# Performance work log

Hardware: AMD Instinct MI355X
Metric: run time of the kernel (lower is better)

Reference implementation:

```python
import jax, jax.numpy as jnp
import numpy as np

N, T, CUT = 64, 2, 25.0            # atoms, atom types, cutoff radius
ED = [3, 32, 64, 128]              # embedding MLP dims (input 3)
LD = [384, 256, 256, 128, 3]       # per-atom MLP dims (input 3*E)
P = T * (T + 1) // 2               # number of unordered type pairs
M = 27 * N                         # periodic images


def setup_inputs() -> dict:
    key = jax.random.key(0)
    ks = jax.random.split(key, 16)
    x = jax.random.uniform(ks[0], (N, 3), jnp.float32) * 10.0
    lattice = 10.0 * jnp.eye(3, dtype=jnp.float32)
    atom_types = (jnp.arange(N) % T).astype(jnp.int32)

    def lin(k, shape, fan_in):
        return jax.random.normal(k, shape, jnp.float32) / np.sqrt(fan_in)

    inp = {"x": x, "lattice": lattice}
    for i in range(3):
        inp[f"We{i+1}"] = lin(ks[1 + i], (P, ED[i], ED[i + 1]), ED[i])
        inp[f"be{i+1}"] = jnp.zeros((P, ED[i + 1]), jnp.float32)
    for i in range(4):
        inp[f"Wl{i+1}"] = lin(ks[5 + i], (N, LD[i], LD[i + 1]), LD[i])
        inp[f"bl{i+1}"] = jnp.zeros((N, LD[i + 1]), jnp.float32)
    inp["atom_types"] = atom_types
    return inp


def reference(x, lattice, We1, be1, We2, be2, We3, be3,
              Wl1, bl1, Wl2, bl2, Wl3, bl3, Wl4, bl4, atom_types):
    act = jax.nn.leaky_relu  # slope 0.01, matches nn.LeakyReLU default
    idx = jnp.arange(-1, 2, dtype=x.dtype)
    # (i,j,k) combos in the same loop order as torch (i slowest, k fastest)
    combos = jnp.stack(jnp.meshgrid(idx, idx, idx, indexing="ij"), -1).reshape(27, 3)
    x_ext = (x[None, :, :] + (combos @ lattice)[:, None, :]).reshape(M, 3)  # [M,3]
    # the in-place subtraction in torch telescopes: at step n, x_ext = x_ext0 - x_ext0[n]
    rel = x_ext[None, :, :] - x_ext[:N, None, :]                    # [N,M,3]
    dist = jnp.linalg.norm(rel, axis=-1)                            # [N,M]
    mask = dist <= CUT
    rank = jnp.cumsum(mask, axis=1) - 1
    # torch removes POSITION n of the compacted neighbor list -> rank == n
    keep = (mask & (rank != jnp.arange(N)[:, None])).astype(x.dtype)  # [N,M]

    types_ext = jnp.tile(atom_types, 27)                            # [M]
    lo = jnp.minimum(atom_types[:, None], types_ext[None, :])
    hi = jnp.maximum(atom_types[:, None], types_ext[None, :])
    pid = lo * T - (lo * (lo - 1)) // 2 + (hi - lo)                 # [N,M] pair-type id

    # run all P pair-type embedding MLPs on every candidate edge, then route
    h = act(jnp.einsum("nmi,pio->pnmo", rel, We1) + be1[:, None, None, :])
    h = act(jnp.einsum("pnmi,pio->pnmo", h, We2) + be2[:, None, None, :])
    h = act(jnp.einsum("pnmi,pio->pnmo", h, We3) + be3[:, None, None, :])
    g = h[pid, jnp.arange(N)[:, None], jnp.arange(M)[None, :], :]   # [N,M,E]

    # d_n = g_n^T @ x_n over kept neighbors; row-major flatten of [E,3] -> [3E]
    d = jnp.einsum("nm,nme,nmc->nec", keep, g, rel).reshape(N, -1)  # [N,3E]

    h = act(jnp.einsum("ni,nio->no", d, Wl1) + bl1)
    h = act(jnp.einsum("ni,nio->no", h, Wl2) + bl2)
    h = act(jnp.einsum("ni,nio->no", h, Wl3) + bl3)
    out = jnp.einsum("ni,nio->no", h, Wl4) + bl4                    # [N,3]
    out = out - jnp.mean(out, axis=0, keepdims=True)
    return out.reshape(-1)                                          # [3N]
```

## Files before the change

kernel.cpp:

```cpp
#include <hip/hip_runtime.h>

#define LEAKY(t) ((t) > 0.0f ? (t) : 0.01f*(t))

typedef __attribute__((ext_vector_type(8))) short short8;
typedef __attribute__((ext_vector_type(4))) float floatx4;

static __device__ __forceinline__ short f2bf(float f) {
  unsigned u = __float_as_uint(f);
  u += 0x7FFFu + ((u >> 16) & 1u);
  return (short)(u >> 16);
}


__global__ __launch_bounds__(256) void prep_kernel(
    const float* __restrict__ We1, const float* __restrict__ be1,
    const float* __restrict__ We2, const float* __restrict__ We3,
    short* __restrict__ g_WT, float* __restrict__ d)
{
  const int gt = blockIdx.x * 256 + threadIdx.x;
  const int GS = gridDim.x * 256;
  for (int i = gt; i < 6144; i += GS) {
    const float4 z = {0.f, 0.f, 0.f, 0.f};
    ((float4*)d)[i] = z;
  }
  for (int it = gt; it < 4224; it += GS) {
    short8 v;
    if (it < 384) {
      const int p = it >> 7, r = it & 127, ot = (r >> 6) & 1, ln = r & 63;
      const int col = ln & 15, quad = ln >> 4, o = ot * 16 + col;
      #pragma unroll
      for (int j = 0; j < 8; ++j) {
        const int k = quad * 8 + j;
        float f = 0.0f;
        if (k < 3) f = We1[p * 96 + k * 32 + o];
        else if (k == 3) f = be1[p * 32 + o];
        v[j] = f2bf(f);
      }
    } else if (it < 1152) {
      const int t = it - 384;
      const int p = t >> 8, r = t & 255, ot = r >> 6, ln = r & 63;
      const int col = ln & 15, quad = ln >> 4, o = ot * 16 + col;
      #pragma unroll
      for (int j = 0; j < 8; ++j) {
        const int k = quad * 8 + j;
        v[j] = f2bf(We2[p * 2048 + k * 64 + o]);
      }
    } else {
      const int t = it - 1152;
      const int p = t >> 10, r = t & 1023, ot = r >> 7, rr = r & 127;
      const int ks = rr >> 6, ln = rr & 63;
      const int col = ln & 15, quad = ln >> 4, o = ot * 16 + col;
      #pragma unroll
      for (int j = 0; j < 8; ++j) {
        const int k = ks * 32 + quad * 8 + j;
        v[j] = f2bf(We3[p * 8192 + k * 128 + o]);
      }
    }
    *(short8*)(g_WT + it * 8) = v;
  }
}

__global__ __launch_bounds__(256, 4) void embed_kernel(
    const float* __restrict__ x, const float* __restrict__ lattice,
    const short* __restrict__ g_WT,
    const float* __restrict__ be2, const float* __restrict__ be3,
    const int* __restrict__ types, float* __restrict__ d)
{
  __shared__ __align__(16) float rel4[144 * 4];
  __shared__ __align__(16) float rk4[144 * 4];
  __shared__ __align__(16) short h1s[144 * 40];
  __shared__ __align__(16) short h2s[144 * 72];

  const int n = blockIdx.x, par = blockIdx.y, chunk = blockIdx.z;
  const int tid = threadIdx.x;
  const int lane = tid & 63, w = tid >> 6;
  const int col = lane & 15, quad = lane >> 4;

  const int tn = types[n];
  const int tj = types[par];
  const int lo = tn < tj ? tn : tj;
  const int hi = tn < tj ? tj : tn;
  const int p  = lo * 2 - (lo * (lo - 1)) / 2 + (hi - lo);

  const short8* WT8 = (const short8*)g_WT;
  const short8 w1b0 = WT8[(p * 2 + 0) * 64 + lane];
  const short8 w1b1 = WT8[(p * 2 + 1) * 64 + lane];
  short8 w2b[4];
  #pragma unroll
  for (int ot = 0; ot < 4; ++ot) w2b[ot] = WT8[384 + (p * 4 + ot) * 64 + lane];
  short8 w3b[2][2];
  #pragma unroll
  for (int nt = 0; nt < 2; ++nt)
    #pragma unroll
    for (int ks = 0; ks < 2; ++ks)
      w3b[nt][ks] = WT8[1152 + ((p * 8 + 2 * w + nt) * 2 + ks) * 64 + lane];
  float bias2[4];
  #pragma unroll
  for (int ot = 0; ot < 4; ++ot) bias2[ot] = be2[p * 64 + ot * 16 + col];
  float bias3[2];
  #pragma unroll
  for (int nt = 0; nt < 2; ++nt) bias3[nt] = be3[p * 128 + w * 32 + nt * 16 + col];

  if (tid < 144) {
    const int q  = chunk * 144 + tid;
    const int c  = q >> 5;
    const int jj = q & 31;
    const int j  = 2 * jj + par;
    const float f0 = (float)(c / 9);
    const float f1 = (float)((c / 3) % 3);
    const float f2c = (float)(c % 3);
    const float rel0 = x[j*3+0] - x[n*3+0] + f0*lattice[0] + f1*lattice[3] + f2c*lattice[6];
    const float rel1 = x[j*3+1] - x[n*3+1] + f0*lattice[1] + f1*lattice[4] + f2c*lattice[7];
    const float rel2 = x[j*3+2] - x[n*3+2] + f0*lattice[2] + f1*lattice[5] + f2c*lattice[8];
    const float dist2 = rel0*rel0 + rel1*rel1 + rel2*rel2;
    const int m = c * 64 + j;
    const bool keep = (dist2 <= 625.0f) && (m != n);
    const float kf = keep ? 1.0f : 0.0f;
    rel4[tid*4+0] = rel0; rel4[tid*4+1] = rel1;
    rel4[tid*4+2] = rel2; rel4[tid*4+3] = 1.0f;
    rk4[tid*4+0] = rel0*kf; rk4[tid*4+1] = rel1*kf;
    rk4[tid*4+2] = rel2*kf; rk4[tid*4+3] = 0.0f;
  }
  __syncthreads();

  for (int mt = w; mt < 9; mt += 4) {
    const float4 r4 = *(const float4*)&rel4[(mt*16 + col) * 4];
    short8 a = {0, 0, 0, 0, 0, 0, 0, 0};
    if (quad == 0) {
      a[0] = f2bf(r4.x); a[1] = f2bf(r4.y); a[2] = f2bf(r4.z);
      a[3] = (short)0x3F80;
    }
    const floatx4 z = {0.f, 0.f, 0.f, 0.f};
    const floatx4 c0 = __builtin_amdgcn_mfma_f32_16x16x32_bf16(a, w1b0, z, 0, 0, 0);
    const floatx4 c1 = __builtin_amdgcn_mfma_f32_16x16x32_bf16(a, w1b1, z, 0, 0, 0);
    #pragma unroll
    for (int r = 0; r < 4; ++r) {
      const int pair = mt*16 + quad*4 + r;
      h1s[pair*40 +      col] = f2bf(LEAKY(c0[r]));
      h1s[pair*40 + 16 + col] = f2bf(LEAKY(c1[r]));
    }
  }
  __syncthreads();

  for (int mt = w; mt < 9; mt += 4) {
    const short8 a = *(const short8*)&h1s[(mt*16 + col) * 40 + quad*8];
    #pragma unroll
    for (int ot = 0; ot < 4; ++ot) {
      floatx4 acc = {bias2[ot], bias2[ot], bias2[ot], bias2[ot]};
      acc = __builtin_amdgcn_mfma_f32_16x16x32_bf16(a, w2b[ot], acc, 0, 0, 0);
      #pragma unroll
      for (int r = 0; r < 4; ++r) {
        const int pair = mt*16 + quad*4 + r;
        h2s[pair*72 + ot*16 + col] = f2bf(LEAKY(acc[r]));
      }
    }
  }
  __syncthreads();

  float vacc[2][3] = {{0,0,0},{0,0,0}};
  for (int mt = 0; mt < 9; ++mt) {
    const short8 a0 = *(const short8*)&h2s[(mt*16 + col) * 72 +      quad*8];
    const short8 a1 = *(const short8*)&h2s[(mt*16 + col) * 72 + 32 + quad*8];
    float4 rks[4];
    #pragma unroll
    for (int r = 0; r < 4; ++r)
      rks[r] = *(const float4*)&rk4[(mt*16 + quad*4 + r) * 4];
    #pragma unroll
    for (int nt = 0; nt < 2; ++nt) {
      floatx4 acc = {bias3[nt], bias3[nt], bias3[nt], bias3[nt]};
      acc = __builtin_amdgcn_mfma_f32_16x16x32_bf16(a0, w3b[nt][0], acc, 0, 0, 0);
      acc = __builtin_amdgcn_mfma_f32_16x16x32_bf16(a1, w3b[nt][1], acc, 0, 0, 0);
      #pragma unroll
      for (int r = 0; r < 4; ++r) {
        const float h3 = LEAKY(acc[r]);
        vacc[nt][0] += h3 * rks[r].x;
        vacc[nt][1] += h3 * rks[r].y;
        vacc[nt][2] += h3 * rks[r].z;
      }
    }
  }
  #pragma unroll
  for (int nt = 0; nt < 2; ++nt)
    #pragma unroll
    for (int c = 0; c < 3; ++c) {
      float v = vacc[nt][c];
      v += __shfl_xor(v, 16, 64);
      v += __shfl_xor(v, 32, 64);
      vacc[nt][c] = v;
    }
  if (lane < 32) {
    const int nts = lane >> 4, colw = lane & 15;
    const int o = w*32 + nts*16 + colw;
    #pragma unroll
    for (int c = 0; c < 3; ++c)
      atomicAdd(&d[n*384 + o*3 + c], nts ? vacc[1][c] : vacc[0][c]);
  }
}

__global__ __launch_bounds__(256) void fit1_kernel(
    const float* __restrict__ d, const float* __restrict__ W,
    const float* __restrict__ b, float* __restrict__ out)
{
  __shared__ float din[384];
  __shared__ floatx4 red[256];
  const int n = blockIdx.x, os = blockIdx.y * 32, tid = threadIdx.x;
  for (int i = tid; i < 384; i += 256) din[i] = d[n*384 + i];
  __syncthreads();
  const int g = tid & 7, s = tid >> 3;
  const float* Wp = W + (size_t)n * 98304 + os + 4 * g;
  floatx4 acc = {0, 0, 0, 0};
  #pragma unroll
  for (int k = 0; k < 12; ++k) {
    const int i = s * 12 + k;
    acc += din[i] * *(const floatx4*)(Wp + (size_t)i * 256);
  }
  red[tid] = acc;
  __syncthreads();
  #pragma unroll
  for (int off = 128; off >= 8; off >>= 1) {
    if (tid < off) red[tid] += red[tid + off];
    __syncthreads();
  }
  if (tid < 8) {
    const floatx4 v = red[tid];
    const int o = os + 4 * tid;
    const float4 bb = *(const float4*)&b[n*256 + o];
    float4 r;
    r.x = LEAKY(v[0] + bb.x); r.y = LEAKY(v[1] + bb.y);
    r.z = LEAKY(v[2] + bb.z); r.w = LEAKY(v[3] + bb.w);
    *(float4*)&out[n*256 + o] = r;
  }
}

__global__ __launch_bounds__(256) void fit2_kernel(
    const float* __restrict__ in, const float* __restrict__ W,
    const float* __restrict__ b, float* __restrict__ out)
{
  __shared__ float din[256];
  __shared__ floatx4 red[256];
  const int n = blockIdx.x, os = blockIdx.y * 32, tid = threadIdx.x;
  din[tid] = in[n*256 + tid];
  __syncthreads();
  const int g = tid & 7, s = tid >> 3;
  const float* Wp = W + (size_t)n * 65536 + os + 4 * g;
  floatx4 acc = {0, 0, 0, 0};
  #pragma unroll
  for (int k = 0; k < 8; ++k) {
    const int i = s * 8 + k;
    acc += din[i] * *(const floatx4*)(Wp + (size_t)i * 256);
  }
  red[tid] = acc;
  __syncthreads();
  #pragma unroll
  for (int off = 128; off >= 8; off >>= 1) {
    if (tid < off) red[tid] += red[tid + off];
    __syncthreads();
  }
  if (tid < 8) {
    const floatx4 v = red[tid];
    const int o = os + 4 * tid;
    const float4 bb = *(const float4*)&b[n*256 + o];
    float4 r;
    r.x = LEAKY(v[0] + bb.x); r.y = LEAKY(v[1] + bb.y);
    r.z = LEAKY(v[2] + bb.z); r.w = LEAKY(v[3] + bb.w);
    *(float4*)&out[n*256 + o] = r;
  }
}

__global__ __launch_bounds__(256) void fit3_kernel(
    const float* __restrict__ in, const float* __restrict__ W,
    const float* __restrict__ b, float* __restrict__ out)
{
  __shared__ float din[256];
  __shared__ floatx4 red[256];
  const int n = blockIdx.x, os = blockIdx.y * 16, tid = threadIdx.x;
  din[tid] = in[n*256 + tid];
  __syncthreads();
  const int g = tid & 3, s = tid >> 2;
  const float* Wp = W + (size_t)n * 32768 + os + 4 * g;
  floatx4 acc = {0, 0, 0, 0};
  #pragma unroll
  for (int k = 0; k < 4; ++k) {
    const int i = s * 4 + k;
    acc += din[i] * *(const floatx4*)(Wp + (size_t)i * 128);
  }
  red[tid] = acc;
  __syncthreads();
  #pragma unroll
  for (int off = 128; off >= 4; off >>= 1) {
    if (tid < off) red[tid] += red[tid + off];
    __syncthreads();
  }
  if (tid < 4) {
    const floatx4 v = red[tid];
    const int o = os + 4 * tid;
    const float4 bb = *(const float4*)&b[n*128 + o];
    float4 r;
    r.x = LEAKY(v[0] + bb.x); r.y = LEAKY(v[1] + bb.y);
    r.z = LEAKY(v[2] + bb.z); r.w = LEAKY(v[3] + bb.w);
    *(float4*)&out[n*128 + o] = r;
  }
}

__global__ __launch_bounds__(256) void fit4_kernel(
    const float* __restrict__ h3, const float* __restrict__ W,
    const float* __restrict__ b, float* __restrict__ out)
{
  __shared__ float part[256 * 3];
  __shared__ float pre[192];
  __shared__ float meanv[3];
  const int tid = threadIdx.x;
  const int n = tid >> 2, q = tid & 3;
  const float* Wn = W + (size_t)n * 384;
  const float* h  = h3 + n * 128;
  float a0 = 0.f, a1 = 0.f, a2 = 0.f;
  for (int k = 0; k < 32; ++k) {
    const int i = q * 32 + k;
    const float hv = h[i];
    a0 += hv * Wn[i*3 + 0];
    a1 += hv * Wn[i*3 + 1];
    a2 += hv * Wn[i*3 + 2];
  }
  part[tid*3+0] = a0; part[tid*3+1] = a1; part[tid*3+2] = a2;
  __syncthreads();
  if (tid < 192) {
    const int nn = tid / 3, o = tid % 3;
    float t = part[(nn*4+0)*3+o] + part[(nn*4+1)*3+o]
            + part[(nn*4+2)*3+o] + part[(nn*4+3)*3+o] + b[tid];
    pre[tid] = t;
  }
  __syncthreads();
  if (tid < 3) {
    float s = 0.f;
    for (int nn = 0; nn < 64; ++nn) s += pre[nn*3 + tid];
    meanv[tid] = s * (1.0f / 64.0f);
  }
  __syncthreads();
  if (tid < 192) out[tid] = pre[tid] - meanv[tid % 3];
}

extern "C" void kernel_launch(void* const* d_in, const int* in_sizes, int n_in,
                              void* d_out, int out_size, void* d_ws, size_t ws_size,
                              hipStream_t stream) {
  const float* x       = (const float*)d_in[0];
  const float* lattice = (const float*)d_in[1];
  const float* We1 = (const float*)d_in[2];
  const float* be1 = (const float*)d_in[3];
  const float* We2 = (const float*)d_in[4];
  const float* be2 = (const float*)d_in[5];
  const float* We3 = (const float*)d_in[6];
  const float* be3 = (const float*)d_in[7];
  const float* Wl1 = (const float*)d_in[8];
  const float* bl1 = (const float*)d_in[9];
  const float* Wl2 = (const float*)d_in[10];
  const float* bl2 = (const float*)d_in[11];
  const float* Wl3 = (const float*)d_in[12];
  const float* bl3 = (const float*)d_in[13];
  const float* Wl4 = (const float*)d_in[14];
  const float* bl4 = (const float*)d_in[15];
  const int*   types = (const int*)d_in[16];

  float* wsf = (float*)d_ws;
  float* dsc  = wsf;
  float* h1f  = wsf + 24576;
  float* h2f  = wsf + 40960;
  float* h3f  = wsf + 57344;
  short* g_WT = (short*)(wsf + 65536);

  prep_kernel<<<32, 256, 0, stream>>>(We1, be1, We2, We3, g_WT, dsc);
  embed_kernel<<<dim3(64, 2, 6), 256, 0, stream>>>(
      x, lattice, g_WT, be2, be3, types, dsc);
  fit1_kernel<<<dim3(64, 8), 256, 0, stream>>>(dsc, Wl1, bl1, h1f);
  fit2_kernel<<<dim3(64, 8), 256, 0, stream>>>(h1f, Wl2, bl2, h2f);
  fit3_kernel<<<dim3(64, 8), 256, 0, stream>>>(h2f, Wl3, bl3, h3f);
  fit4_kernel<<<1, 256, 0, stream>>>(h3f, Wl4, bl4, (float*)d_out);
}
```

Measured before the change: 140.6 us.

## Fuse per-atom MLP layers into one kernel and replace atomics with partial-sum slots

The four separate fitting-MLP kernels are merged into a single per-atom kernel with 512 threads that keeps the intermediate activations in shared memory, plus a small mean kernel. The embedding kernel now writes per-(pair, chunk) partial results into 12 slots instead of doing atomicAdd, so the zeroing pass in prep is dropped and the fit kernel sums the slots. This removes launches, global round-trips of activations and atomic contention. In exchange the fit stage runs on only 64 blocks, where each layer previously used 512 blocks, so weight-streaming parallelism drops.

```diff
diff --git a/kernel.cpp b/kernel.cpp
--- a/kernel.cpp
+++ b/kernel.cpp
@@ -15,14 +15,10 @@
 __global__ __launch_bounds__(256) void prep_kernel(
     const float* __restrict__ We1, const float* __restrict__ be1,
     const float* __restrict__ We2, const float* __restrict__ We3,
-    short* __restrict__ g_WT, float* __restrict__ d)
+    short* __restrict__ g_WT)
 {
   const int gt = blockIdx.x * 256 + threadIdx.x;
   const int GS = gridDim.x * 256;
-  for (int i = gt; i < 6144; i += GS) {
-    const float4 z = {0.f, 0.f, 0.f, 0.f};
-    ((float4*)d)[i] = z;
-  }
   for (int it = gt; it < 4224; it += GS) {
     short8 v;
     if (it < 384) {
@@ -64,7 +60,7 @@
     const float* __restrict__ x, const float* __restrict__ lattice,
     const short* __restrict__ g_WT,
     const float* __restrict__ be2, const float* __restrict__ be3,
-    const int* __restrict__ types, float* __restrict__ d)
+    const int* __restrict__ types, float* __restrict__ dpart)
 {
   __shared__ __align__(16) float rel4[144 * 4];
   __shared__ __align__(16) float rk4[144 * 4];
@@ -191,152 +187,151 @@
   if (lane < 32) {
     const int nts = lane >> 4, colw = lane & 15;
     const int o = w*32 + nts*16 + colw;
+    const int slot = par * 6 + chunk;
+    float* dst = dpart + ((size_t)(slot * 64 + n)) * 384 + o * 3;
     #pragma unroll
     for (int c = 0; c < 3; ++c)
-      atomicAdd(&d[n*384 + o*3 + c], nts ? vacc[1][c] : vacc[0][c]);
-  }
-}
-
-__global__ __launch_bounds__(256) void fit1_kernel(
-    const float* __restrict__ d, const float* __restrict__ W,
-    const float* __restrict__ b, float* __restrict__ out)
+      dst[c] = nts ? vacc[1][c] : vacc[0][c];
+  }
+}
+
+__global__ __launch_bounds__(512) void fit_kernel(
+    const float* __restrict__ dpart,
+    const float* __restrict__ W1, const float* __restrict__ b1,
+    const float* __restrict__ W2, const float* __restrict__ b2,
+    const float* __restrict__ W3, const float* __restrict__ b3,
+    const float* __restrict__ W4, const float* __restrict__ b4,
+    float* __restrict__ pre)
 {
-  __shared__ float din[384];
-  __shared__ floatx4 red[256];
-  const int n = blockIdx.x, os = blockIdx.y * 32, tid = threadIdx.x;
-  for (int i = tid; i < 384; i += 256) din[i] = d[n*384 + i];
-  __syncthreads();
-  const int g = tid & 7, s = tid >> 3;
-  const float* Wp = W + (size_t)n * 98304 + os + 4 * g;
-  floatx4 acc = {0, 0, 0, 0};
-  #pragma unroll
-  for (int k = 0; k < 12; ++k) {
-    const int i = s * 12 + k;
-    acc += din[i] * *(const floatx4*)(Wp + (size_t)i * 256);
-  }
-  red[tid] = acc;
-  __syncthreads();
-  #pragma unroll
-  for (int off = 128; off >= 8; off >>= 1) {
-    if (tid < off) red[tid] += red[tid + off];
-    __syncthreads();
-  }
-  if (tid < 8) {
-    const floatx4 v = red[tid];
-    const int o = os + 4 * tid;
-    const float4 bb = *(const float4*)&b[n*256 + o];
-    float4 r;
-    r.x = LEAKY(v[0] + bb.x); r.y = LEAKY(v[1] + bb.y);
-    r.z = LEAKY(v[2] + bb.z); r.w = LEAKY(v[3] + bb.w);
-    *(float4*)&out[n*256 + o] = r;
-  }
-}
-
-__global__ __launch_bounds__(256) void fit2_kernel(
-    const float* __restrict__ in, const float* __restrict__ W,
-    const float* __restrict__ b, float* __restrict__ out)
+  __shared__ __align__(16) float a0[384];
+  __shared__ __align__(16) float a1[256];
+  __shared__ __align__(16) float a2[256];
+  __shared__ __align__(16) float a3[128];
+  __shared__ __align__(16) floatx4 red[512];
+  const int n = blockIdx.x, tid = threadIdx.x;
+
+  for (int i = tid; i < 384; i += 512) {
+    float s = 0.f;
+    #pragma unroll
+    for (int sl = 0; sl < 12; ++sl)
+      s += dpart[((size_t)(sl * 64 + n)) * 384 + i];
+    a0[i] = s;
+  }
+  __syncthreads();
+
+  {
+    const int g = tid & 63, s = tid >> 6;
+    const float* Wp = W1 + (size_t)n * 98304 + 4 * g;
+    floatx4 acc = {0.f, 0.f, 0.f, 0.f};
+    #pragma unroll 16
+    for (int k = 0; k < 48; ++k) {
+      const int i = s * 48 + k;
+      acc += a0[i] * *(const floatx4*)(Wp + (size_t)i * 256);
+    }
+    red[tid] = acc;
+    __syncthreads();
+    if (tid < 64) {
+      floatx4 v = red[tid];
+      #pragma unroll
+      for (int s2 = 1; s2 < 8; ++s2) v += red[s2 * 64 + tid];
+      const float4 bb = *(const float4*)&b1[n * 256 + 4 * tid];
+      a1[4*tid+0] = LEAKY(v[0] + bb.x);
+      a1[4*tid+1] = LEAKY(v[1] + bb.y);
+      a1[4*tid+2] = LEAKY(v[2] + bb.z);
+      a1[4*tid+3] = LEAKY(v[3] + bb.w);
+    }
+    __syncthreads();
+  }
+
+  {
+    const int g = tid & 63, s = tid >> 6;
+    const float* Wp = W2 + (size_t)n * 65536 + 4 * g;
+    floatx4 acc = {0.f, 0.f, 0.f, 0.f};
+    #pragma unroll 16
+    for (int k = 0; k < 32; ++k) {
+      const int i = s * 32 + k;
+      acc += a1[i] * *(const floatx4*)(Wp + (size_t)i * 256);
+    }
+    red[tid] = acc;
+    __syncthreads();
+    if (tid < 64) {
+      floatx4 v = red[tid];
+      #pragma unroll
+      for (int s2 = 1; s2 < 8; ++s2) v += red[s2 * 64 + tid];
+      const float4 bb = *(const float4*)&b2[n * 256 + 4 * tid];
+      a2[4*tid+0] = LEAKY(v[0] + bb.x);
+      a2[4*tid+1] = LEAKY(v[1] + bb.y);
+      a2[4*tid+2] = LEAKY(v[2] + bb.z);
+      a2[4*tid+3] = LEAKY(v[3] + bb.w);
+    }
+    __syncthreads();
+  }
+
+  {
+    const int g = tid & 31, s = tid >> 5;
+    const float* Wp = W3 + (size_t)n * 32768 + 4 * g;
+    floatx4 acc = {0.f, 0.f, 0.f, 0.f};
+    #pragma unroll
+    for (int k = 0; k < 16; ++k) {
+      const int i = s * 16 + k;
+      acc += a2[i] * *(const floatx4*)(Wp + (size_t)i * 128);
+    }
+    red[tid] = acc;
+    __syncthreads();
+    if (tid < 32) {
+      floatx4 v = red[tid];
+      #pragma unroll
+      for (int s2 = 1; s2 < 16; ++s2) v += red[s2 * 32 + tid];
+      const float4 bb = *(const float4*)&b3[n * 128 + 4 * tid];
+      a3[4*tid+0] = LEAKY(v[0] + bb.x);
+      a3[4*tid+1] = LEAKY(v[1] + bb.y);
+      a3[4*tid+2] = LEAKY(v[2] + bb.z);
+      a3[4*tid+3] = LEAKY(v[3] + bb.w);
+    }
+    __syncthreads();
+  }
+
+  {
+    float* redf = (float*)red;
+    if (tid < 128) {
+      const float hv = a3[tid];
+      const float* W4n = W4 + (size_t)n * 384;
+      float p0 = hv * W4n[tid*3 + 0];
+      float p1 = hv * W4n[tid*3 + 1];
+      float p2 = hv * W4n[tid*3 + 2];
+      #pragma unroll
+      for (int off = 32; off >= 1; off >>= 1) {
+        p0 += __shfl_down(p0, off, 64);
+        p1 += __shfl_down(p1, off, 64);
+        p2 += __shfl_down(p2, off, 64);
+      }
+      if ((tid & 63) == 0) {
+        const int wv = tid >> 6;
+        redf[wv*3 + 0] = p0; redf[wv*3 + 1] = p1; redf[wv*3 + 2] = p2;
+      }
+    }
+    __syncthreads();
+    if (tid < 3)
+      pre[n*3 + tid] = redf[tid] + redf[3 + tid] + b4[n*3 + tid];
+  }
+}
+
+__global__ __launch_bounds__(256) void mean_kernel(
+    const float* __restrict__ pre, float* __restrict__ out)
 {
-  __shared__ float din[256];
-  __shared__ floatx4 red[256];
-  const int n = blockIdx.x, os = blockIdx.y * 32, tid = threadIdx.x;
-  din[tid] = in[n*256 + tid];
-  __syncthreads();
-  const int g = tid & 7, s = tid >> 3;
-  const float* Wp = W + (size_t)n * 65536 + os + 4 * g;
-  floatx4 acc = {0, 0, 0, 0};
-  #pragma unroll
-  for (int k = 0; k < 8; ++k) {
-    const int i = s * 8 + k;
-    acc += din[i] * *(const floatx4*)(Wp + (size_t)i * 256);
-  }
-  red[tid] = acc;
-  __syncthreads();
-  #pragma unroll
-  for (int off = 128; off >= 8; off >>= 1) {
-    if (tid < off) red[tid] += red[tid + off];
-    __syncthreads();
-  }
-  if (tid < 8) {
-    const floatx4 v = red[tid];
-    const int o = os + 4 * tid;
-    const float4 bb = *(const float4*)&b[n*256 + o];
-    float4 r;
-    r.x = LEAKY(v[0] + bb.x); r.y = LEAKY(v[1] + bb.y);
-    r.z = LEAKY(v[2] + bb.z); r.w = LEAKY(v[3] + bb.w);
-    *(float4*)&out[n*256 + o] = r;
-  }
-}
-
-__global__ __launch_bounds__(256) void fit3_kernel(
-    const float* __restrict__ in, const float* __restrict__ W,
-    const float* __restrict__ b, float* __restrict__ out)
-{
-  __shared__ float din[256];
-  __shared__ floatx4 red[256];
-  const int n = blockIdx.x, os = blockIdx.y * 16, tid = threadIdx.x;
-  din[tid] = in[n*256 + tid];
-  __syncthreads();
-  const int g = tid & 3, s = tid >> 2;
-  const float* Wp = W + (size_t)n * 32768 + os + 4 * g;
-  floatx4 acc = {0, 0, 0, 0};
-  #pragma unroll
-  for (int k = 0; k < 4; ++k) {
-    const int i = s * 4 + k;
-    acc += din[i] * *(const floatx4*)(Wp + (size_t)i * 128);
-  }
-  red[tid] = acc;
-  __syncthreads();
-  #pragma unroll
-  for (int off = 128; off >= 4; off >>= 1) {
-    if (tid < off) red[tid] += red[tid + off];
-    __syncthreads();
-  }
-  if (tid < 4) {
-    const floatx4 v = red[tid];
-    const int o = os + 4 * tid;
-    const float4 bb = *(const float4*)&b[n*128 + o];
-    float4 r;
-    r.x = LEAKY(v[0] + bb.x); r.y = LEAKY(v[1] + bb.y);
-    r.z = LEAKY(v[2] + bb.z); r.w = LEAKY(v[3] + bb.w);
-    *(float4*)&out[n*128 + o] = r;
-  }
-}
-
-__global__ __launch_bounds__(256) void fit4_kernel(
-    const float* __restrict__ h3, const float* __restrict__ W,
-    const float* __restrict__ b, float* __restrict__ out)
-{
-  __shared__ float part[256 * 3];
-  __shared__ float pre[192];
+  __shared__ float sp[192];
   __shared__ float meanv[3];
   const int tid = threadIdx.x;
-  const int n = tid >> 2, q = tid & 3;
-  const float* Wn = W + (size_t)n * 384;
-  const float* h  = h3 + n * 128;
-  float a0 = 0.f, a1 = 0.f, a2 = 0.f;
-  for (int k = 0; k < 32; ++k) {
-    const int i = q * 32 + k;
-    const float hv = h[i];
-    a0 += hv * Wn[i*3 + 0];
-    a1 += hv * Wn[i*3 + 1];
-    a2 += hv * Wn[i*3 + 2];
-  }
-  part[tid*3+0] = a0; part[tid*3+1] = a1; part[tid*3+2] = a2;
-  __syncthreads();
-  if (tid < 192) {
-    const int nn = tid / 3, o = tid % 3;
-    float t = part[(nn*4+0)*3+o] + part[(nn*4+1)*3+o]
-            + part[(nn*4+2)*3+o] + part[(nn*4+3)*3+o] + b[tid];
-    pre[tid] = t;
-  }
+  if (tid < 192) sp[tid] = pre[tid];
   __syncthreads();
   if (tid < 3) {
     float s = 0.f;
-    for (int nn = 0; nn < 64; ++nn) s += pre[nn*3 + tid];
+    #pragma unroll
+    for (int nn = 0; nn < 64; ++nn) s += sp[nn*3 + tid];
     meanv[tid] = s * (1.0f / 64.0f);
   }
   __syncthreads();
-  if (tid < 192) out[tid] = pre[tid] - meanv[tid % 3];
+  if (tid < 192) out[tid] = sp[tid] - meanv[tid % 3];
 }
 
 extern "C" void kernel_launch(void* const* d_in, const int* in_sizes, int n_in,
@@ -360,18 +355,15 @@
   const float* bl4 = (const float*)d_in[15];
   const int*   types = (const int*)d_in[16];
 
-  float* wsf = (float*)d_ws;
-  float* dsc  = wsf;
-  float* h1f  = wsf + 24576;
-  float* h2f  = wsf + 40960;
-  float* h3f  = wsf + 57344;
-  short* g_WT = (short*)(wsf + 65536);
-
-  prep_kernel<<<32, 256, 0, stream>>>(We1, be1, We2, We3, g_WT, dsc);
+  float* wsf   = (float*)d_ws;
+  float* dpart = wsf;
+  float* pre   = wsf + 294912;
+  short* g_WT  = (short*)(wsf + 295104);
+
+  prep_kernel<<<17, 256, 0, stream>>>(We1, be1, We2, We3, g_WT);
   embed_kernel<<<dim3(64, 2, 6), 256, 0, stream>>>(
-      x, lattice, g_WT, be2, be3, types, dsc);
-  fit1_kernel<<<dim3(64, 8), 256, 0, stream>>>(dsc, Wl1, bl1, h1f);
-  fit2_kernel<<<dim3(64, 8), 256, 0, stream>>>(h1f, Wl2, bl2, h2f);
-  fit3_kernel<<<dim3(64, 8), 256, 0, stream>>>(h2f, Wl3, bl3, h3f);
-  fit4_kernel<<<1, 256, 0, stream>>>(h3f, Wl4, bl4, (float*)d_out);
-}
+      x, lattice, g_WT, be2, be3, types, dpart);
+  fit_kernel<<<64, 512, 0, stream>>>(
+      dpart, Wl1, bl1, Wl2, bl2, Wl3, bl3, Wl4, bl4, pre);
+  mean_kernel<<<1, 256, 0, stream>>>(pre, (float*)d_out);
+}
```

New measurement: 131.5 us. 6.5% less time.
